# Optimization experiments

Hardware: AMD Instinct MI355X
Metric: run time of the kernel (lower is better)

## Reference

```python
import jax, jax.numpy as jnp
import numpy as np

NUM_NODES_G1 = 60000
NUM_NODES_G2 = 50000
NUM_REL = 16
NUM_BASES = 4
DIM = 128  # node_dim == hidden_dim == final_dim
L_COMMON = 100


def _concept_layer(x, edge_index):
    # Gather-based concept propagation: x_i <- x_i + mean_{j in N(i)} x_j
    src, dst = edge_index[0], edge_index[1]
    n = x.shape[0]
    agg = jax.ops.segment_sum(x[src], dst, num_segments=n)
    deg = jax.ops.segment_sum(jnp.ones((src.shape[0],), x.dtype), dst, num_segments=n)
    return x + agg / jnp.clip(deg, 1.0)[:, None]


def _rgcn_layer(x, edge_index, edge_type, basis, comp, root, bias):
    # Basis-decomposed RGCN: out_i = x_i @ root + bias + sum_r (1/|N_i^r|) sum_{j in N_i^r} x_j @ W_r,
    # W_r = sum_b comp[r,b] * basis[b]. Reorder: scatter comp-weighted x[src] per basis, then one GEMM per basis.
    src, dst = edge_index[0], edge_index[1]
    n = x.shape[0]
    e = src.shape[0]
    seg = dst * NUM_REL + edge_type  # per-(node, relation) bucket
    cnt = jax.ops.segment_sum(jnp.ones((e,), x.dtype), seg, num_segments=n * NUM_REL)
    norm = 1.0 / jnp.clip(cnt, 1.0)
    coef = comp[edge_type] * norm[seg][:, None]  # [E, B]
    xsrc = x[src]  # [E, D] -- dominant gather traffic
    out = x @ root + bias
    for b in range(NUM_BASES):  # small fixed loop over bases
        agg_b = jax.ops.segment_sum(xsrc * coef[:, b:b + 1], dst, num_segments=n)
        out = out + agg_b @ basis[b]
    return out


def setup_inputs() -> dict:
    key = jax.random.key(0)
    ks = jax.random.split(key, 16)
    e2, e1 = 800000, 800000
    return {
        "edge_index_g2": jax.random.randint(ks[0], (2, e2), 0, NUM_NODES_G2),
        "edge_type_g2": jax.random.randint(ks[1], (e2,), 0, NUM_REL),
        "edge_index_g1": jax.random.randint(ks[2], (2, e1), 0, NUM_NODES_G1),
        "left_common": jax.random.randint(ks[3], (L_COMMON,), 0, NUM_NODES_G1),
        "all_node_embedding": jax.random.normal(ks[4], (NUM_NODES_G1, DIM), jnp.float32),
        "basis1": jax.random.normal(ks[5], (NUM_BASES, DIM, DIM), jnp.float32) * 0.05,
        "comp1": jax.random.normal(ks[6], (NUM_REL, NUM_BASES), jnp.float32),
        "root1": jax.random.normal(ks[7], (DIM, DIM), jnp.float32) * 0.05,
        "bias1": jnp.zeros((DIM,), jnp.float32),
        "basis2": jax.random.normal(ks[8], (NUM_BASES, DIM, DIM), jnp.float32) * 0.05,
        "comp2": jax.random.normal(ks[9], (NUM_REL, NUM_BASES), jnp.float32),
        "root2": jax.random.normal(ks[10], (DIM, DIM), jnp.float32) * 0.05,
        "bias2": jnp.zeros((DIM,), jnp.float32),
        "weights": jax.random.uniform(ks[11], (DIM, 1), jnp.float32),
    }


def reference(edge_index_g2, edge_type_g2, edge_index_g1, left_common,
              all_node_embedding, basis1, comp1, root1, bias1,
              basis2, comp2, root2, bias2, weights):
    x_g1 = jax.nn.relu(_concept_layer(all_node_embedding, edge_index_g1))
    x = x_g1[:NUM_NODES_G2]
    x = _rgcn_layer(x, edge_index_g2, edge_type_g2, basis1, comp1, root1, bias1)
    x = jax.nn.relu(x)  # relu_use == 1
    x_g2 = _rgcn_layer(x, edge_index_g2, edge_type_g2, basis2, comp2, root2, bias2)
    ty = x_g1[left_common]  # [L, D]
    # mul_def outer elementwise product followed by matmul with weights collapses to one contraction:
    # logits[n,l] = sum_d x_g2[n,d] * ty[l,d] * w[d]
    logits = jnp.einsum('nd,ld,d->nl', x_g2, ty, weights[:, 0])
    return jax.nn.softmax(logits, axis=1)
```

## Files before the change

kernel.cpp:

```cpp
#include <hip/hip_runtime.h>
#include <hip/hip_bf16.h>
#include <math.h>

#define N1 60000
#define N2 50000
#define DIM 128
#define NREL 16
#define NB 4
#define LCOM 100
#define LPAD 112
#define NPART 8
#define NC 64

typedef __attribute__((ext_vector_type(8))) short short8;
typedef __attribute__((ext_vector_type(4))) float f32x4;
typedef __attribute__((ext_vector_type(4))) _Float16 half4;
typedef __attribute__((ext_vector_type(8))) _Float16 half8;

__device__ __forceinline__ float bf2f(unsigned short u) {
    union { unsigned int i; float f; } c; c.i = ((unsigned int)u) << 16; return c.f;
}
__device__ __forceinline__ unsigned short f2bf(float f) {
    union { float f; unsigned int i; } c; c.f = f;
    unsigned int r = c.i + 0x7FFF + ((c.i >> 16) & 1);
    return (unsigned short)(r >> 16);
}
__device__ __forceinline__ void split8(float4 a, float4 b, short8& h, short8& l) {
    float f[8] = {a.x, a.y, a.z, a.w, b.x, b.y, b.z, b.w};
#pragma unroll
    for (int j = 0; j < 8; j++) {
        unsigned short hh = f2bf(f[j]);
        h[j] = (short)hh;
        l[j] = (short)f2bf(f[j] - bf2f(hh));
    }
}

__global__ __launch_bounds__(256) void k_prelude(
        const int* __restrict__ ei1, int E1, int* __restrict__ degs1,
        const int* __restrict__ ei2, int E2, int* __restrict__ degs2,
        const float* __restrict__ root1, const float* __restrict__ basis1,
        unsigned short* __restrict__ Wh1, unsigned short* __restrict__ Wl1,
        const float* __restrict__ root2, const float* __restrict__ basis2,
        unsigned short* __restrict__ Wh2, unsigned short* __restrict__ Wl2, int PB,
        const float* __restrict__ emb, _Float16* __restrict__ embh, int n4) {
    __shared__ int hist[7500];
    int b = blockIdx.x;
    const int HB = NPART * NC;
    if (b < 2 * HB) {
        int isg2 = b >= HB;
        int bb = isg2 ? b - HB : b;
        int p = bb & (NPART - 1);
        int c = bb >> 3;
        const int* dsts = isg2 ? ei2 + E2 : ei1 + E1;
        int E = isg2 ? E2 : E1;
        int N = isg2 ? N2 : N1;
        int* degs = isg2 ? degs2 : degs1;
        const int W = (N + NPART - 1) / NPART;
        int lo = p * W, hi = min(lo + W, N);
        int span = hi - lo;
        for (int i = threadIdx.x; i < span; i += 256) hist[i] = 0;
        __syncthreads();
        int chunk = (E + NC - 1) / NC;
        int e0 = c * chunk, e1 = min(e0 + chunk, E);
        for (int base = e0; base < e1; base += 1024) {
            int d[4]; bool ok[4];
#pragma unroll
            for (int j = 0; j < 4; j++) {
                int e = base + threadIdx.x + j * 256;
                bool inb = e < e1;
                d[j] = inb ? __builtin_nontemporal_load(dsts + e) : -1;
                ok[j] = inb && d[j] >= lo && d[j] < hi;
            }
#pragma unroll
            for (int j = 0; j < 4; j++)
                if (ok[j]) atomicAdd(&hist[d[j] - lo], 1);
        }
        __syncthreads();
        int* slice = degs + (size_t)c * N + lo;
        for (int i = threadIdx.x; i < span; i += 256) slice[i] = hist[i];
    } else if (b < 2 * HB + PB) {
        int t = (b - 2 * HB) * 256 + threadIdx.x;
        if (t < 2 * 640 * 128) {
            int which = t >= 640 * 128;
            int tt = which ? t - 640 * 128 : t;
            const float* root = which ? root2 : root1;
            const float* basis = which ? basis2 : basis1;
            unsigned short* Wh = which ? Wh2 : Wh1;
            unsigned short* Wl = which ? Wl2 : Wl1;
            int k = tt >> 7, n = tt & 127;
            float v = (k < 128) ? root[k * 128 + n] : basis[(k - 128) * 128 + n];
            unsigned short h = f2bf(v);
            Wh[n * 640 + k] = h;
            Wl[n * 640 + k] = f2bf(v - bf2f(h));
        }
    } else {
        int i = (b - 2 * HB - PB) * 256 + threadIdx.x;
        if (i < n4) {
            float4 v = ((const float4*)emb)[i];
            half4 o = {(_Float16)v.x, (_Float16)v.y, (_Float16)v.z, (_Float16)v.w};
            ((half4*)embh)[i] = o;
        }
    }
}

__global__ __launch_bounds__(256) void k_scan_p1m(const int* __restrict__ degsA, int* __restrict__ degA,
                                                  int nA, int nbA, int* __restrict__ bsumA,
                                                  const int* __restrict__ degsB, int* __restrict__ degB,
                                                  int nB, int* __restrict__ bsumB) {
    __shared__ int red[256];
    const int* degs; int* deg; int n; int* bsum; int b;
    if ((int)blockIdx.x < nbA) { degs = degsA; deg = degA; n = nA; bsum = bsumA; b = blockIdx.x; }
    else { degs = degsB; deg = degB; n = nB; bsum = bsumB; b = blockIdx.x - nbA; }
    int base = b * 1024;
    int tid = threadIdx.x;
    int s = 0;
#pragma unroll
    for (int j = 0; j < 4; j++) {
        int i = base + tid + j * 256;
        if (i < n) {
            int v = 0;
            for (int c = 0; c < NC; c++) v += degs[(size_t)c * n + i];
            deg[i] = v;
            s += v;
        }
    }
    red[tid] = s;
    __syncthreads();
    for (int d = 128; d; d >>= 1) {
        if (tid < d) red[tid] += red[tid + d];
        __syncthreads();
    }
    if (tid == 0) bsum[b] = red[0];
}

__global__ __launch_bounds__(64) void k_scan_p2m(const int* __restrict__ bsumA, int* __restrict__ boffA,
                                                 int* __restrict__ offA, int nbA, int nA,
                                                 const int* __restrict__ bsumB, int* __restrict__ boffB,
                                                 int* __restrict__ offB, int nbB, int nB) {
    __shared__ int s[64];
    const int* bsum; int* boff; int* off; int nb; int n;
    if (blockIdx.x == 0) { bsum = bsumA; boff = boffA; off = offA; nb = nbA; n = nA; }
    else { bsum = bsumB; boff = boffB; off = offB; nb = nbB; n = nB; }
    int tid = threadIdx.x;
    int v = (tid < nb) ? bsum[tid] : 0;
    s[tid] = v;
    __syncthreads();
    for (int d = 1; d < 64; d <<= 1) {
        int t = (tid >= d) ? s[tid - d] : 0;
        __syncthreads();
        s[tid] += t;
        __syncthreads();
    }
    if (tid < nb) boff[tid] = s[tid] - v;
    if (tid == 63) off[n] = s[63];
}

__global__ __launch_bounds__(256) void k_scan_p3m(const int* __restrict__ inA, const int* __restrict__ boffA,
                                                  int* __restrict__ offA, int* __restrict__ sbA,
                                                  int nA, int nbA,
                                                  const int* __restrict__ inB, const int* __restrict__ boffB,
                                                  int* __restrict__ offB, int* __restrict__ sbB, int nB) {
    __shared__ int red[256];
    const int* in; const int* boff; int* off; int* sb; int n; int b;
    if ((int)blockIdx.x < nbA) { in = inA; boff = boffA; off = offA; sb = sbA; n = nA; b = blockIdx.x; }
    else { in = inB; boff = boffB; off = offB; sb = sbB; n = nB; b = blockIdx.x - nbA; }
    int base = b * 1024;
    int tid = threadIdx.x;
    int v[4];
    int s = 0;
#pragma unroll
    for (int j = 0; j < 4; j++) {
        int i = base + tid * 4 + j;
        v[j] = (i < n) ? in[i] : 0;
        s += v[j];
    }
    red[tid] = s;
    __syncthreads();
    for (int d = 1; d < 256; d <<= 1) {
        int t = (tid >= d) ? red[tid - d] : 0;
        __syncthreads();
        red[tid] += t;
        __syncthreads();
    }
    int run = boff[b] + red[tid] - s;
#pragma unroll
    for (int j = 0; j < 4; j++) {
        int i = base + tid * 4 + j;
        if (i < n) {
            off[i] = run;
            run += v[j];
        }
    }
    __syncthreads();
    for (int i = base + tid; i < min(base + 1024, n); i += 256) {
        int run2 = off[i];
        for (int c = 0; c < NC; c++) {
            size_t idx = (size_t)c * n + i;
            int t = sb[idx];
            sb[idx] = run2;
            run2 += t;
        }
    }
}

__global__ __launch_bounds__(256) void k_scat(const int* __restrict__ ei1, int E1,
                                              const int* __restrict__ sb1, int* __restrict__ elist1,
                                              const int* __restrict__ ei2, const int* __restrict__ et2,
                                              int E2, const int* __restrict__ sb2, int* __restrict__ elist2) {
    __shared__ int lcur[7500];
    int b = blockIdx.x;
    const int HB = NPART * NC;
    int isg2 = b >= HB;
    int bb = isg2 ? b - HB : b;
    int p = bb & (NPART - 1);
    int c = bb >> 3;
    const int* ei = isg2 ? ei2 : ei1;
    int E = isg2 ? E2 : E1;
    int N = isg2 ? N2 : N1;
    const int* sb = isg2 ? sb2 : sb1;
    int* elist = isg2 ? elist2 : elist1;
    const int W = (N + NPART - 1) / NPART;
    int lo = p * W, hi = min(lo + W, N);
    int span = hi - lo;
    for (int i = threadIdx.x; i < span; i += 256) lcur[i] = 0;
    __syncthreads();
    const int* sbc = sb + (size_t)c * N;
    int chunk = (E + NC - 1) / NC;
    int e0 = c * chunk, e1 = min(e0 + chunk, E);
    for (int base = e0; base < e1; base += 1024) {
        int d[4], sv[4], tv[4]; bool ok[4];
#pragma unroll
        for (int j = 0; j < 4; j++) {
            int e = base + threadIdx.x + j * 256;
            bool inb = e < e1;
            d[j] = inb ? __builtin_nontemporal_load(ei + E + e) : -1;
            sv[j] = inb ? __builtin_nontemporal_load(ei + e) : 0;
            tv[j] = (inb && isg2) ? __builtin_nontemporal_load(et2 + e) : 0;
            ok[j] = inb && d[j] >= lo && d[j] < hi;
        }
#pragma unroll
        for (int j = 0; j < 4; j++) {
            if (ok[j]) {
                int li = atomicAdd(&lcur[d[j] - lo], 1);
                int pay = isg2 ? ((sv[j] << 4) | tv[j]) : sv[j];
                elist[sbc[d[j]] + li] = pay;
            }
        }
    }
}

__global__ __launch_bounds__(256) void k_mix(
        const _Float16* __restrict__ embh, const float* __restrict__ emb,
        const int* __restrict__ off1, const int* __restrict__ elist1,
        float* __restrict__ xg1, _Float16* __restrict__ xg1h, int CONC_B,
        const int* __restrict__ lc, const float* __restrict__ w,
        unsigned short* __restrict__ tyh, unsigned short* __restrict__ tyl) {
    int b = blockIdx.x;
    if (b < CONC_B) {
        int node = b * 4 + (threadIdx.x >> 6);
        int lane = threadIdx.x & 63;
        if (node >= N2) return;
        int quad = lane >> 4, d8 = (lane & 15) * 8;
        int s0 = off1[node], s1 = off1[node + 1];
        float acc[8] = {};
        int i = s0;
#define CLOAD(P) (*(const half8*)(embh + (size_t)(P) * DIM + d8))
        for (; i + 16 <= s1; i += 16) {
            int q0 = elist1[i + quad];
            int q1 = elist1[i + 4 + quad];
            int q2 = elist1[i + 8 + quad];
            int q3 = elist1[i + 12 + quad];
            half8 h0 = CLOAD(q0), h1 = CLOAD(q1), h2 = CLOAD(q2), h3 = CLOAD(q3);
#pragma unroll
            for (int j = 0; j < 8; j++) acc[j] += (float)h0[j] + (float)h1[j];
#pragma unroll
            for (int j = 0; j < 8; j++) acc[j] += (float)h2[j] + (float)h3[j];
        }
        if (i + 8 <= s1) {
            int q0 = elist1[i + quad];
            int q1 = elist1[i + 4 + quad];
            half8 h0 = CLOAD(q0), h1 = CLOAD(q1);
#pragma unroll
            for (int j = 0; j < 8; j++) acc[j] += (float)h0[j] + (float)h1[j];
            i += 8;
        }
        if (i + 4 <= s1) {
            int q0 = elist1[i + quad];
            half8 h0 = CLOAD(q0);
#pragma unroll
            for (int j = 0; j < 8; j++) acc[j] += (float)h0[j];
            i += 4;
        }
        if (i < s1) {
            int e = i + quad;
            bool ok = e < s1;
            int q0 = elist1[ok ? e : i];
            half8 h0 = CLOAD(q0);
            if (ok) {
#pragma unroll
                for (int j = 0; j < 8; j++) acc[j] += (float)h0[j];
            }
        }
#undef CLOAD
#pragma unroll
        for (int j = 0; j < 8; j++) {
            acc[j] += __shfl_xor(acc[j], 16, 64);
            acc[j] += __shfl_xor(acc[j], 32, 64);
        }
        if (quad == 0) {
            float inv = 1.0f / (float)max(s1 - s0, 1);
            const float* ep = emb + (size_t)node * DIM + d8;
            float4 e0 = *(const float4*)(ep);
            float4 e1 = *(const float4*)(ep + 4);
            float o[8];
            o[0] = fmaxf(e0.x + acc[0] * inv, 0.f);
            o[1] = fmaxf(e0.y + acc[1] * inv, 0.f);
            o[2] = fmaxf(e0.z + acc[2] * inv, 0.f);
            o[3] = fmaxf(e0.w + acc[3] * inv, 0.f);
            o[4] = fmaxf(e1.x + acc[4] * inv, 0.f);
            o[5] = fmaxf(e1.y + acc[5] * inv, 0.f);
            o[6] = fmaxf(e1.z + acc[6] * inv, 0.f);
            o[7] = fmaxf(e1.w + acc[7] * inv, 0.f);
            float4 w0 = {o[0], o[1], o[2], o[3]};
            float4 w1 = {o[4], o[5], o[6], o[7]};
            *(float4*)(xg1 + (size_t)node * DIM + d8) = w0;
            *(float4*)(xg1 + (size_t)node * DIM + d8 + 4) = w1;
            half8 oh;
#pragma unroll
            for (int j = 0; j < 8; j++) oh[j] = (_Float16)o[j];
            *(half8*)(xg1h + (size_t)node * DIM + d8) = oh;
        }
    } else {
        if (threadIdx.x >= 64) return;
        int l = b - CONC_B;
        int lane = threadIdx.x;
        int d0 = lane * 2;
        if (l >= LCOM) {
            ushort2 z = {0, 0};
            *(ushort2*)(tyh + (size_t)l * 128 + d0) = z;
            *(ushort2*)(tyl + (size_t)l * 128 + d0) = z;
            return;
        }
        int row = lc[l];
        int s0 = off1[row], s1 = off1[row + 1];
        float2 acc = {0.f, 0.f};
        for (int i = s0; i < s1; i++) {
            int s = elist1[i];
            float2 v = *(const float2*)(emb + (size_t)s * DIM + lane * 2);
            acc.x += v.x; acc.y += v.y;
        }
        float inv = 1.0f / (float)max(s1 - s0, 1);
        float2 e = *(const float2*)(emb + (size_t)row * DIM + lane * 2);
        float v0 = fmaxf(e.x + acc.x * inv, 0.f) * w[d0];
        float v1 = fmaxf(e.y + acc.y * inv, 0.f) * w[d0 + 1];
        unsigned short h0 = f2bf(v0), h1 = f2bf(v1);
        ushort2 hh = {h0, h1};
        ushort2 ll = {f2bf(v0 - bf2f(h0)), f2bf(v1 - bf2f(h1))};
        *(ushort2*)(tyh + (size_t)l * 128 + d0) = hh;
        *(ushort2*)(tyl + (size_t)l * 128 + d0) = ll;
    }
}

__global__ __launch_bounds__(256) void k_rgcn_gather(const _Float16* __restrict__ xh,
                                                     const int* __restrict__ off,
                                                     const int* __restrict__ elist,
                                                     const float* __restrict__ comp,
                                                     _Float16* __restrict__ aggh, int n) {
    __shared__ float scomp[NREL * NB];
    __shared__ float nrmlds[4][NREL];
    if (threadIdx.x < NREL * NB) scomp[threadIdx.x] = comp[threadIdx.x];
    __syncthreads();
    int nb = threadIdx.x >> 6;
    int node = blockIdx.x * 4 + nb;
    int lane = threadIdx.x & 63;
    if (node >= n) return;
    int s0 = off[node], s1 = off[node + 1];
    unsigned long long c0 = 0, c1 = 0;
    for (int i = s0 + lane; i < s1; i += 64) {
        int t = elist[i] & 15;
        if (t < 8) c0 += 1ull << (8 * t); else c1 += 1ull << (8 * (t - 8));
    }
#pragma unroll
    for (int o = 32; o; o >>= 1) {
        c0 += __shfl_xor(c0, o, 64);
        c1 += __shfl_xor(c1, o, 64);
    }
    if (lane < NREL) {
        unsigned int c = (lane < 8) ? (unsigned int)((c0 >> (8 * lane)) & 255)
                                    : (unsigned int)((c1 >> (8 * (lane - 8))) & 255);
        nrmlds[nb][lane] = 1.0f / (float)max(c, 1u);
    }
    int quad = lane >> 4, d8 = (lane & 15) * 8;
    float a[4][8] = {};
#define RGE(P, GATE)                                                           \
    {                                                                          \
        int s_ = (P) >> 4, t_ = (P) & 15;                                      \
        float nr_ = nrmlds[nb][t_] * (GATE);                                   \
        float4 cf_ = *(const float4*)(scomp + t_ * 4);                         \
        half8 hv_ = *(const half8*)(xh + (size_t)s_ * DIM + d8);               \
        float c0_ = cf_.x * nr_, c1_ = cf_.y * nr_;                            \
        float c2_ = cf_.z * nr_, c3_ = cf_.w * nr_;                            \
        _Pragma("unroll")                                                      \
        for (int j = 0; j < 8; j++) {                                          \
            float v_ = (float)hv_[j];                                          \
            a[0][j] = fmaf(c0_, v_, a[0][j]);                                  \
            a[1][j] = fmaf(c1_, v_, a[1][j]);                                  \
            a[2][j] = fmaf(c2_, v_, a[2][j]);                                  \
            a[3][j] = fmaf(c3_, v_, a[3][j]);                                  \
        }                                                                      \
    }
    int i = s0;
    for (; i + 8 <= s1; i += 8) {
        int pa = elist[i + quad];
        int pb = elist[i + 4 + quad];
        RGE(pa, 1.0f);
        RGE(pb, 1.0f);
    }
    if (i + 4 <= s1) {
        int pa = elist[i + quad];
        RGE(pa, 1.0f);
        i += 4;
    }
    if (i < s1) {
        int e = i + quad;
        bool ok = e < s1;
        int pa = elist[ok ? e : i];
        RGE(pa, ok ? 1.0f : 0.0f);
    }
#undef RGE
#pragma unroll
    for (int bb = 0; bb < 4; bb++)
#pragma unroll
        for (int j = 0; j < 8; j++) {
            a[bb][j] += __shfl_xor(a[bb][j], 16, 64);
            a[bb][j] += __shfl_xor(a[bb][j], 32, 64);
        }
    if (quad == 0) {
        _Float16* o = aggh + (size_t)node * (NB * DIM) + d8;
#pragma unroll
        for (int bb = 0; bb < 4; bb++) {
            half8 hv;
#pragma unroll
            for (int j = 0; j < 8; j++) hv[j] = (_Float16)a[bb][j];
            *(half8*)(o + bb * DIM) = hv;
        }
    }
}

#define LDSK 40
__global__ __launch_bounds__(256) void k_gemm(const float* __restrict__ x,
                                              const _Float16* __restrict__ aggh,
                                              const unsigned short* __restrict__ Wh,
                                              const unsigned short* __restrict__ Wl,
                                              const float* __restrict__ bias,
                                              float* __restrict__ out,
                                              _Float16* __restrict__ out_h, int relu) {
    __shared__ __align__(16) short Ah[128 * LDSK];
    __shared__ __align__(16) short Al[128 * LDSK];
    __shared__ __align__(16) short Bh[128 * LDSK];
    __shared__ __align__(16) short Bl[128 * LDSK];
    int tid = threadIdx.x;
    int lane = tid & 63, wid = tid >> 6;
    int wave_m = wid >> 1, wave_n = wid & 1;
    int l15 = lane & 15, quad = lane >> 4;
    int row0 = blockIdx.x * 128;

    int srow = tid >> 1, skh = (tid & 1) * 16;

    f32x4 acc[4][4] = {};
    for (int k0 = 0; k0 < 640; k0 += 32) {
        {
            int rg = row0 + srow;
            float4 q0 = {0, 0, 0, 0}, q1 = q0, q2 = q0, q3 = q0;
            if (rg < N2) {
                if (k0 < 128) {
                    const float* src = x + (size_t)rg * 128 + k0 + skh;
                    q0 = *(const float4*)(src + 0);
                    q1 = *(const float4*)(src + 4);
                    q2 = *(const float4*)(src + 8);
                    q3 = *(const float4*)(src + 12);
                } else {
                    const _Float16* src = aggh + (size_t)rg * 512 + (k0 - 128) + skh;
                    half8 ha = *(const half8*)(src);
                    half8 hb = *(const half8*)(src + 8);
                    q0 = {(float)ha[0], (float)ha[1], (float)ha[2], (float)ha[3]};
                    q1 = {(float)ha[4], (float)ha[5], (float)ha[6], (float)ha[7]};
                    q2 = {(float)hb[0], (float)hb[1], (float)hb[2], (float)hb[3]};
                    q3 = {(float)hb[4], (float)hb[5], (float)hb[6], (float)hb[7]};
                }
            }
            short8 h0, l0, h1, l1;
            split8(q0, q1, h0, l0);
            split8(q2, q3, h1, l1);
            *(short8*)(&Ah[srow * LDSK + skh]) = h0;
            *(short8*)(&Ah[srow * LDSK + skh + 8]) = h1;
            *(short8*)(&Al[srow * LDSK + skh]) = l0;
            *(short8*)(&Al[srow * LDSK + skh + 8]) = l1;
        }
        {
            const unsigned short* sh = Wh + (size_t)srow * 640 + k0 + skh;
            const unsigned short* sl = Wl + (size_t)srow * 640 + k0 + skh;
            *(short8*)(&Bh[srow * LDSK + skh]) = *(const short8*)(sh);
            *(short8*)(&Bh[srow * LDSK + skh + 8]) = *(const short8*)(sh + 8);
            *(short8*)(&Bl[srow * LDSK + skh]) = *(const short8*)(sl);
            *(short8*)(&Bl[srow * LDSK + skh + 8]) = *(const short8*)(sl + 8);
        }
        __syncthreads();
        short8 ah[4], al[4], bh[4], bl[4];
#pragma unroll
        for (int i = 0; i < 4; i++) {
            int ro = (wave_m * 64 + i * 16 + l15) * LDSK + quad * 8;
            ah[i] = *(const short8*)(&Ah[ro]);
            al[i] = *(const short8*)(&Al[ro]);
        }
#pragma unroll
        for (int j = 0; j < 4; j++) {
            int ro = (wave_n * 64 + j * 16 + l15) * LDSK + quad * 8;
            bh[j] = *(const short8*)(&Bh[ro]);
            bl[j] = *(const short8*)(&Bl[ro]);
        }
#pragma unroll
        for (int i = 0; i < 4; i++)
#pragma unroll
            for (int j = 0; j < 4; j++) {
                acc[i][j] = __builtin_amdgcn_mfma_f32_16x16x32_bf16(al[i], bh[j], acc[i][j], 0, 0, 0);
                acc[i][j] = __builtin_amdgcn_mfma_f32_16x16x32_bf16(ah[i], bl[j], acc[i][j], 0, 0, 0);
                acc[i][j] = __builtin_amdgcn_mfma_f32_16x16x32_bf16(ah[i], bh[j], acc[i][j], 0, 0, 0);
            }
        __syncthreads();
    }
#pragma unroll
    for (int j = 0; j < 4; j++) {
        int gcol = wave_n * 64 + j * 16 + l15;
        float bv = bias[gcol];
#pragma unroll
        for (int i = 0; i < 4; i++) {
            int grow_base = row0 + wave_m * 64 + i * 16 + quad * 4;
#pragma unroll
            for (int r = 0; r < 4; r++) {
                int grow = grow_base + r;
                if (grow >= N2) continue;
                float v = acc[i][j][r] + bv;
                if (relu) v = fmaxf(v, 0.f);
                out[(size_t)grow * 128 + gcol] = v;
                if (out_h) out_h[(size_t)grow * 128 + gcol] = (_Float16)v;
            }
        }
    }
}

__global__ __launch_bounds__(256) void k_logits(const float* __restrict__ h2,
                                                const unsigned short* __restrict__ tyh,
                                                const unsigned short* __restrict__ tyl,
                                                float* __restrict__ out, int M) {
    int wid = threadIdx.x >> 6, lane = threadIdx.x & 63;
    int l15 = lane & 15, quad = lane >> 4;
    int row0w = blockIdx.x * 64 + wid * 16;
    int arow = min(row0w + l15, M - 1);
    f32x4 acc[7] = {};
#pragma unroll
    for (int k0 = 0; k0 < 128; k0 += 32) {
        const float* ap = h2 + (size_t)arow * 128 + k0 + quad * 8;
        float4 q0 = *(const float4*)(ap);
        float4 q1 = *(const float4*)(ap + 4);
        short8 ah, al;
        split8(q0, q1, ah, al);
#pragma unroll
        for (int j = 0; j < 7; j++) {
            size_t bo = (size_t)(j * 16 + l15) * 128 + k0 + quad * 8;
            short8 bh = *(const short8*)(tyh + bo);
            short8 bl = *(const short8*)(tyl + bo);
            acc[j] = __builtin_amdgcn_mfma_f32_16x16x32_bf16(al, bh, acc[j], 0, 0, 0);
            acc[j] = __builtin_amdgcn_mfma_f32_16x16x32_bf16(ah, bl, acc[j], 0, 0, 0);
            acc[j] = __builtin_amdgcn_mfma_f32_16x16x32_bf16(ah, bh, acc[j], 0, 0, 0);
        }
    }
    bool v6 = (l15 < LCOM - 96);
#pragma unroll
    for (int r = 0; r < 4; r++) {
        int grow = row0w + quad * 4 + r;
        float m = -INFINITY;
#pragma unroll
        for (int j = 0; j < 6; j++) m = fmaxf(m, acc[j][r]);
        if (v6) m = fmaxf(m, acc[6][r]);
        m = fmaxf(m, __shfl_xor(m, 8, 64));
        m = fmaxf(m, __shfl_xor(m, 4, 64));
        m = fmaxf(m, __shfl_xor(m, 2, 64));
        m = fmaxf(m, __shfl_xor(m, 1, 64));
        float e[7];
        float s = 0.f;
#pragma unroll
        for (int j = 0; j < 6; j++) { e[j] = __expf(acc[j][r] - m); s += e[j]; }
        e[6] = v6 ? __expf(acc[6][r] - m) : 0.f;
        s += e[6];
        s += __shfl_xor(s, 8, 64);
        s += __shfl_xor(s, 4, 64);
        s += __shfl_xor(s, 2, 64);
        s += __shfl_xor(s, 1, 64);
        float inv = 1.0f / s;
        if (grow < M) {
#pragma unroll
            for (int j = 0; j < 6; j++) out[(size_t)grow * LCOM + j * 16 + l15] = e[j] * inv;
            if (v6) out[(size_t)grow * LCOM + 96 + l15] = e[6] * inv;
        }
    }
}

extern "C" void kernel_launch(void* const* d_in, const int* in_sizes, int n_in,
                              void* d_out, int out_size, void* d_ws, size_t ws_size,
                              hipStream_t stream) {
    const int* ei2 = (const int*)d_in[0];
    const int* et2 = (const int*)d_in[1];
    const int* ei1 = (const int*)d_in[2];
    const int* lc = (const int*)d_in[3];
    const float* emb = (const float*)d_in[4];
    const float* basis1 = (const float*)d_in[5];
    const float* comp1 = (const float*)d_in[6];
    const float* root1 = (const float*)d_in[7];
    const float* bias1 = (const float*)d_in[8];
    const float* basis2 = (const float*)d_in[9];
    const float* comp2 = (const float*)d_in[10];
    const float* root2 = (const float*)d_in[11];
    const float* bias2 = (const float*)d_in[12];
    const float* wts = (const float*)d_in[13];
    float* out = (float*)d_out;
    int E2 = in_sizes[0] / 2, E1 = in_sizes[2] / 2;

    float* ws = (float*)d_ws;
    float* xg1 = ws;
    float* h1 = xg1 + 6400000;
    float* agg = h1 + 6400000;
    _Float16* emb_h = (_Float16*)(agg + 25600000);
    unsigned short* tyh = (unsigned short*)(emb_h + 7680000);
    unsigned short* tyl = tyh + LPAD * 128;
    unsigned short* Wh1 = tyl + LPAD * 128;
    unsigned short* Wl1 = Wh1 + 81920;
    unsigned short* Wh2 = Wl1 + 81920;
    unsigned short* Wl2 = Wh2 + 81920;
    int* ipool = (int*)(Wl2 + 81920);
    int* deg1 = ipool;
    int* deg2 = deg1 + 60000;
    int* off1 = deg2 + 50000;
    int* elist1 = off1 + 60001;
    int* off2 = elist1 + 800000;
    int* elist2 = off2 + 50001;
    int* bsum1 = elist2 + 800000;
    int* boff1 = bsum1 + 64;
    int* bsum2 = boff1 + 64;
    int* boff2 = bsum2 + 64;
    int* degs1 = (int*)agg;
    int* degs2 = degs1 + NC * N1;
    _Float16* agg_h = (_Float16*)agg;
    _Float16* xg1_h = (_Float16*)h1;
    _Float16* h1_h = emb_h;
    float* h2 = xg1;

    const int NB1 = (N1 + 1023) / 1024;
    const int NB2 = (N2 + 1023) / 1024;
    const int PB = (2 * 640 * 128) / 256;
    const int CB = (N1 * DIM / 4 + 255) / 256;
    const int CONC_B = (N2 + 3) / 4;

    k_prelude<<<2 * NPART * NC + PB + CB, 256, 0, stream>>>(
        ei1, E1, degs1, ei2, E2, degs2,
        root1, basis1, Wh1, Wl1, root2, basis2, Wh2, Wl2, PB,
        emb, emb_h, N1 * DIM / 4);

    k_scan_p1m<<<NB1 + NB2, 256, 0, stream>>>(degs1, deg1, N1, NB1, bsum1,
                                              degs2, deg2, N2, bsum2);
    k_scan_p2m<<<2, 64, 0, stream>>>(bsum1, boff1, off1, NB1, N1, bsum2, boff2, off2, NB2, N2);
    k_scan_p3m<<<NB1 + NB2, 256, 0, stream>>>(deg1, boff1, off1, degs1, N1, NB1,
                                              deg2, boff2, off2, degs2, N2);

    k_scat<<<2 * NPART * NC, 256, 0, stream>>>(ei1, E1, degs1, elist1,
                                               ei2, et2, E2, degs2, elist2);

    k_mix<<<CONC_B + LPAD, 256, 0, stream>>>(
        emb_h, emb, off1, elist1, xg1, xg1_h, CONC_B,
        lc, wts, tyh, tyl);

    k_rgcn_gather<<<CONC_B, 256, 0, stream>>>(xg1_h, off2, elist2, comp1, agg_h, N2);
    k_gemm<<<(N2 + 127) / 128, 256, 0, stream>>>(xg1, agg_h, Wh1, Wl1, bias1, h1, h1_h, 1);

    k_rgcn_gather<<<CONC_B, 256, 0, stream>>>(h1_h, off2, elist2, comp2, agg_h, N2);
    k_gemm<<<(N2 + 127) / 128, 256, 0, stream>>>(h1, agg_h, Wh2, Wl2, bias2, h2, (_Float16*)nullptr, 0);

    k_logits<<<(N2 + 63) / 64, 256, 0, stream>>>(h2, tyh, tyl, out, N2);
}
```

Measured before the change: 527.2 us.

## Overlap second-half RGCN gather with first-half GEMM in a combined kernel

Each RGCN layer's node range is split at a fixed row boundary. The first half is gathered by a standalone kernel. A combined kernel then runs the second-half gather blocks alongside the GEMM blocks for the first half, and a final GEMM kernel covers the remaining rows. The aim is to fill the GPU during the gather-to-GEMM dependency gap and hide the memory-bound gather behind compute. In exchange it adds launches per layer, and the combined kernel's gather blocks reserve the GEMM's larger LDS, which can lower occupancy for the gather work.

```diff
diff --git a/kernel.cpp b/kernel.cpp
--- a/kernel.cpp
+++ b/kernel.cpp
@@ -11,6 +11,7 @@
 #define LPAD 112
 #define NPART 8
 #define NC 64
+#define HSPLIT 25088
 
 typedef __attribute__((ext_vector_type(8))) short short8;
 typedef __attribute__((ext_vector_type(4))) float f32x4;
@@ -361,19 +362,18 @@
     }
 }
 
-__global__ __launch_bounds__(256) void k_rgcn_gather(const _Float16* __restrict__ xh,
-                                                     const int* __restrict__ off,
-                                                     const int* __restrict__ elist,
-                                                     const float* __restrict__ comp,
-                                                     _Float16* __restrict__ aggh, int n) {
-    __shared__ float scomp[NREL * NB];
-    __shared__ float nrmlds[4][NREL];
+__device__ __forceinline__ void gather_dev(
+        int bid, int nbase, int nend,
+        const _Float16* __restrict__ xh, const int* __restrict__ off,
+        const int* __restrict__ elist, const float* __restrict__ comp,
+        _Float16* __restrict__ aggh,
+        float* scomp, float (*nrmlds)[NREL]) {
     if (threadIdx.x < NREL * NB) scomp[threadIdx.x] = comp[threadIdx.x];
     __syncthreads();
     int nb = threadIdx.x >> 6;
-    int node = blockIdx.x * 4 + nb;
+    int node = nbase + bid * 4 + nb;
     int lane = threadIdx.x & 63;
-    if (node >= n) return;
+    if (node >= nend) return;
     int s0 = off[node], s1 = off[node + 1];
     unsigned long long c0 = 0, c1 = 0;
     for (int i = s0 + lane; i < s1; i += 64) {
@@ -448,22 +448,18 @@
 }
 
 #define LDSK 40
-__global__ __launch_bounds__(256) void k_gemm(const float* __restrict__ x,
-                                              const _Float16* __restrict__ aggh,
-                                              const unsigned short* __restrict__ Wh,
-                                              const unsigned short* __restrict__ Wl,
-                                              const float* __restrict__ bias,
-                                              float* __restrict__ out,
-                                              _Float16* __restrict__ out_h, int relu) {
-    __shared__ __align__(16) short Ah[128 * LDSK];
-    __shared__ __align__(16) short Al[128 * LDSK];
-    __shared__ __align__(16) short Bh[128 * LDSK];
-    __shared__ __align__(16) short Bl[128 * LDSK];
+__device__ __forceinline__ void gemm_dev(
+        int rblk,
+        const float* __restrict__ x, const _Float16* __restrict__ aggh,
+        const unsigned short* __restrict__ Wh, const unsigned short* __restrict__ Wl,
+        const float* __restrict__ bias, float* __restrict__ out,
+        _Float16* __restrict__ out_h, int relu,
+        short* Ah, short* Al, short* Bh, short* Bl) {
     int tid = threadIdx.x;
     int lane = tid & 63, wid = tid >> 6;
     int wave_m = wid >> 1, wave_n = wid & 1;
     int l15 = lane & 15, quad = lane >> 4;
-    int row0 = blockIdx.x * 128;
+    int row0 = rblk * 128;
 
     int srow = tid >> 1, skh = (tid & 1) * 16;
 
@@ -549,6 +545,52 @@
     }
 }
 
+__global__ __launch_bounds__(256) void k_rgcn_gather(const _Float16* __restrict__ xh,
+                                                     const int* __restrict__ off,
+                                                     const int* __restrict__ elist,
+                                                     const float* __restrict__ comp,
+                                                     _Float16* __restrict__ aggh,
+                                                     int nbase, int nend) {
+    __shared__ float scomp[NREL * NB];
+    __shared__ float nrmlds[4][NREL];
+    gather_dev(blockIdx.x, nbase, nend, xh, off, elist, comp, aggh, scomp, nrmlds);
+}
+
+__global__ __launch_bounds__(256) void k_gemm(const float* __restrict__ x,
+                                              const _Float16* __restrict__ aggh,
+                                              const unsigned short* __restrict__ Wh,
+                                              const unsigned short* __restrict__ Wl,
+                                              const float* __restrict__ bias,
+                                              float* __restrict__ out,
+                                              _Float16* __restrict__ out_h, int relu, int rb0) {
+    __shared__ __align__(16) short Ah[128 * LDSK];
+    __shared__ __align__(16) short Al[128 * LDSK];
+    __shared__ __align__(16) short Bh[128 * LDSK];
+    __shared__ __align__(16) short Bl[128 * LDSK];
+    gemm_dev(rb0 + blockIdx.x, x, aggh, Wh, Wl, bias, out, out_h, relu, Ah, Al, Bh, Bl);
+}
+
+__global__ __launch_bounds__(256) void k_gg(
+        const _Float16* __restrict__ xh, const int* __restrict__ off,
+        const int* __restrict__ elist, const float* __restrict__ comp,
+        _Float16* __restrict__ aggh, int nbase, int nend, int GB,
+        const float* __restrict__ x,
+        const unsigned short* __restrict__ Wh, const unsigned short* __restrict__ Wl,
+        const float* __restrict__ bias, float* __restrict__ out,
+        _Float16* __restrict__ out_h, int relu) {
+    __shared__ float scomp[NREL * NB];
+    __shared__ float nrmlds[4][NREL];
+    __shared__ __align__(16) short Ah[128 * LDSK];
+    __shared__ __align__(16) short Al[128 * LDSK];
+    __shared__ __align__(16) short Bh[128 * LDSK];
+    __shared__ __align__(16) short Bl[128 * LDSK];
+    if ((int)blockIdx.x < GB) {
+        gather_dev(blockIdx.x, nbase, nend, xh, off, elist, comp, aggh, scomp, nrmlds);
+    } else {
+        gemm_dev(blockIdx.x - GB, x, aggh, Wh, Wl, bias, out, out_h, relu, Ah, Al, Bh, Bl);
+    }
+}
+
 __global__ __launch_bounds__(256) void k_logits(const float* __restrict__ h2,
                                                 const unsigned short* __restrict__ tyh,
                                                 const unsigned short* __restrict__ tyl,
@@ -660,6 +702,10 @@
     const int PB = (2 * 640 * 128) / 256;
     const int CB = (N1 * DIM / 4 + 255) / 256;
     const int CONC_B = (N2 + 3) / 4;
+    const int GB1 = HSPLIT / 4;
+    const int GB2 = (N2 - HSPLIT + 3) / 4;
+    const int MB1 = HSPLIT / 128;
+    const int MB2 = (N2 + 127) / 128 - MB1;
 
     k_prelude<<<2 * NPART * NC + PB + CB, 256, 0, stream>>>(
         ei1, E1, degs1, ei2, E2, degs2,
@@ -679,11 +725,15 @@
         emb_h, emb, off1, elist1, xg1, xg1_h, CONC_B,
         lc, wts, tyh, tyl);
 
-    k_rgcn_gather<<<CONC_B, 256, 0, stream>>>(xg1_h, off2, elist2, comp1, agg_h, N2);
-    k_gemm<<<(N2 + 127) / 128, 256, 0, stream>>>(xg1, agg_h, Wh1, Wl1, bias1, h1, h1_h, 1);
-
-    k_rgcn_gather<<<CONC_B, 256, 0, stream>>>(h1_h, off2, elist2, comp2, agg_h, N2);
-    k_gemm<<<(N2 + 127) / 128, 256, 0, stream>>>(h1, agg_h, Wh2, Wl2, bias2, h2, (_Float16*)nullptr, 0);
+    k_rgcn_gather<<<GB1, 256, 0, stream>>>(xg1_h, off2, elist2, comp1, agg_h, 0, HSPLIT);
+    k_gg<<<GB2 + MB1, 256, 0, stream>>>(xg1_h, off2, elist2, comp1, agg_h, HSPLIT, N2, GB2,
+                                        xg1, Wh1, Wl1, bias1, h1, h1_h, 1);
+    k_gemm<<<MB2, 256, 0, stream>>>(xg1, agg_h, Wh1, Wl1, bias1, h1, h1_h, 1, MB1);
+
+    k_rgcn_gather<<<GB1, 256, 0, stream>>>(h1_h, off2, elist2, comp2, agg_h, 0, HSPLIT);
+    k_gg<<<GB2 + MB1, 256, 0, stream>>>(h1_h, off2, elist2, comp2, agg_h, HSPLIT, N2, GB2,
+                                        h1, Wh2, Wl2, bias2, h2, (_Float16*)nullptr, 0);
+    k_gemm<<<MB2, 256, 0, stream>>>(h1, agg_h, Wh2, Wl2, bias2, h2, (_Float16*)nullptr, 0, MB1);
 
     k_logits<<<(N2 + 63) / 64, 256, 0, stream>>>(h2, tyh, tyl, out, N2);
 }
```

Measured after the change: 632.1 us. 19.9% more time.
